# Kernel tuning notes

Hardware: AMD Instinct MI355X
Metric: run time of the kernel (lower is better)

## Reference

```python
import jax, jax.numpy as jnp
import numpy as np

B, L = 2, 1024
D_MODEL = 1024
D_STATE = 16
K = 3            # conv kernel (odd so padding=(K-1)//2 preserves L)
EXPAND = 1       # module is only shape-consistent with d_inner == d_model
D_INNER = D_MODEL * EXPAND


def setup_inputs() -> dict:
    key = jax.random.key(0)
    ks = jax.random.split(key, 10)
    s = 0.02
    x = jax.random.normal(ks[0], (B, L, D_MODEL), dtype=jnp.float32)
    W_in = jax.random.normal(ks[1], (D_MODEL, 2 * D_INNER), dtype=jnp.float32) * s
    conv_w = jax.random.normal(ks[2], (D_INNER, 1, K), dtype=jnp.float32) * s  # depthwise OIH
    W_B = jax.random.normal(ks[3], (D_INNER, D_STATE), dtype=jnp.float32) * s
    W_C = jax.random.normal(ks[4], (D_INNER, D_STATE), dtype=jnp.float32) * s
    W_delta = jax.random.normal(ks[5], (D_INNER, D_MODEL), dtype=jnp.float32) * s
    delta_base = jax.random.normal(ks[6], (D_MODEL,), dtype=jnp.float32)
    W_tau = jax.random.normal(ks[7], (D_MODEL, D_MODEL), dtype=jnp.float32) * s
    A_log = jnp.tile(jnp.log(jnp.arange(1, D_STATE + 1, dtype=jnp.float32)), (D_MODEL, 1))
    W_out = jax.random.normal(ks[8], (D_INNER, D_MODEL), dtype=jnp.float32) * s
    return {"x": x, "W_in": W_in, "conv_w": conv_w, "W_B": W_B, "W_C": W_C,
            "W_delta": W_delta, "delta_base": delta_base, "W_tau": W_tau,
            "A_log": A_log, "W_out": W_out}


def _silu(v):
    return v * jax.nn.sigmoid(v)


def _mamba_fwd(x, W_in, conv_w, W_B, W_C, W_delta, delta_base, W_tau, A_log, W_out):
    residual = x
    z = x @ W_in                               # [B,L,2*D_INNER]
    val, gate = jnp.split(z, 2, axis=-1)
    # depthwise causal-ish conv1d (padding=(K-1)//2)
    v = jnp.transpose(val, (0, 2, 1))          # [B,C,L]
    v = jax.lax.conv_general_dilated(
        v, conv_w, window_strides=(1,), padding=[((K - 1) // 2, (K - 1) // 2)],
        dimension_numbers=("NCH", "OIH", "NCH"), feature_group_count=D_INNER)
    val = jnp.transpose(_silu(v), (0, 2, 1))   # [B,L,D_INNER]

    B_proj = val @ W_B                          # [B,L,N]
    C_proj = val @ W_C                          # [B,L,N]
    combined_delta = val @ W_delta + delta_base # [B,L,D_MODEL]
    Delta = jax.nn.softplus(combined_delta @ W_tau)  # [B,L,D]

    A = -jnp.exp(A_log)                         # [D,N]
    dA = Delta[..., None] * A                   # [B,L,D,N]
    A_bar = jnp.exp(dA)
    B_bar = jnp.expm1(dA) / (dA + 1e-6) * Delta[..., None] * B_proj[:, :, None, :]

    def step(h, inp):
        a_t, b_t, c_t, u_t = inp                # a/b:[B,D,N], c:[B,N], u:[B,D]
        h = a_t * h + b_t * u_t[..., None]
        y_t = jnp.sum(h * c_t[:, None, :], axis=-1)  # [B,D]
        return h, y_t

    h0 = jnp.zeros((x.shape[0], D_INNER, D_STATE), dtype=x.dtype)
    xs = (jnp.moveaxis(A_bar, 1, 0), jnp.moveaxis(B_bar, 1, 0),
          jnp.moveaxis(C_proj, 1, 0), jnp.moveaxis(val, 1, 0))
    _, ys = jax.lax.scan(step, h0, xs)          # ys: [L,B,D]
    y = jnp.moveaxis(ys, 0, 1)                  # [B,L,D]

    out = (y * _silu(gate)) @ W_out + residual  # [B,L,D_MODEL]
    return out


def reference(x, W_in, conv_w, W_B, W_C, W_delta, delta_base, W_tau, A_log, W_out):
    return _mamba_fwd(x, W_in, conv_w, W_B, W_C, W_delta, delta_base, W_tau, A_log, W_out)
```

## Files before the change

kernel.cpp:

```cpp
#include <hip/hip_runtime.h>
#include <math.h>

#define BB 2
#define LL 1024
#define DM 1024
#define DI 1024
#define DS 16
#define ROWS (BB * LL)
#define CH 16
#define NCH (LL / CH)
#define NP 1152

typedef unsigned short ushort_t;
typedef __attribute__((ext_vector_type(8))) short short8;
typedef __attribute__((ext_vector_type(4))) float f32x4;
typedef __attribute__((ext_vector_type(4))) float f4;
typedef __attribute__((ext_vector_type(4))) ushort_t us4;

static __device__ __forceinline__ float sp_f(float x) {
    return fmaxf(x, 0.f) + log1pf(expf(-fabsf(x)));
}
static __device__ __forceinline__ ushort_t f2bf(float f) {
    unsigned u = __float_as_uint(f);
    u += 0x7fffu + ((u >> 16) & 1u);
    return (ushort_t)(u >> 16);
}
static __device__ __forceinline__ float bf2f(ushort_t s) {
    return __uint_as_float(((unsigned)s) << 16);
}

#define SWZ(L) ((L) ^ ((((L) >> 7) & 1) << 4) ^ ((((L) >> 8) & 1) << 5))

template <int ACT, bool HAS_BIAS, bool HAS_RES, bool OUTBF, bool PROJ>
__global__ __launch_bounds__(256) void gemm_bf_k(
    const ushort_t* __restrict__ A, const ushort_t* __restrict__ Bt,
    const float* __restrict__ bias, const float* __restrict__ res,
    void* __restrict__ Cout, float* __restrict__ BpO, float* __restrict__ CpO,
    int M, int N, int K)
{
    __shared__ __align__(16) char lsa[8192];
    __shared__ __align__(16) char lsb[8192];

    const int tid = threadIdx.x;
    const int lane = tid & 63;
    const int w = tid >> 6, wr = w >> 1, wc = w & 1;
    const int row0 = blockIdx.y * 128, col0 = blockIdx.x * 128;
    const int rl = lane & 15, q = lane >> 4;

    const int srow = tid >> 2, schunk = tid & 3;
    const int Pw0 = SWZ(tid * 16);
    const int Pw1 = SWZ(4096 + tid * 16);

    int LA[4], LB[4];
#pragma unroll
    for (int m = 0; m < 4; ++m) LA[m] = SWZ((wr * 64 + m * 16 + rl) * 64 + q * 16);
#pragma unroll
    for (int n = 0; n < 4; ++n) LB[n] = SWZ((wc * 64 + n * 16 + rl) * 64 + q * 16);

    const ushort_t* pA = A + (size_t)(row0 + srow) * K + schunk * 8;
    const ushort_t* pB = Bt + (size_t)(col0 + srow) * K + schunk * 8;
    const size_t rowskip = (size_t)64 * K;

    short8 ra0 = *(const short8*)(pA);
    short8 ra1 = *(const short8*)(pA + rowskip);
    short8 rb0 = *(const short8*)(pB);
    short8 rb1 = *(const short8*)(pB + rowskip);

    f32x4 acc[4][4] = {};

    const int NT = K >> 5;
    for (int kt = 0; kt < NT; ++kt) {
        __syncthreads();
        *(short8*)(lsa + Pw0) = ra0;
        *(short8*)(lsa + Pw1) = ra1;
        *(short8*)(lsb + Pw0) = rb0;
        *(short8*)(lsb + Pw1) = rb1;
        __syncthreads();
        if (kt + 1 < NT) {
            const ushort_t* nA = pA + (size_t)(kt + 1) * 32;
            const ushort_t* nB = pB + (size_t)(kt + 1) * 32;
            ra0 = *(const short8*)(nA);
            ra1 = *(const short8*)(nA + rowskip);
            rb0 = *(const short8*)(nB);
            rb1 = *(const short8*)(nB + rowskip);
        }
        short8 af[4], bfr[4];
#pragma unroll
        for (int m = 0; m < 4; ++m) af[m] = *(const short8*)(lsa + LA[m]);
#pragma unroll
        for (int n = 0; n < 4; ++n) bfr[n] = *(const short8*)(lsb + LB[n]);
#pragma unroll
        for (int m = 0; m < 4; ++m)
#pragma unroll
            for (int n = 0; n < 4; ++n)
                acc[m][n] = __builtin_amdgcn_mfma_f32_16x16x32_bf16(
                    af[m], bfr[n], acc[m][n], 0, 0, 0);
    }

    float bia[4];
#pragma unroll
    for (int n = 0; n < 4; ++n) {
        int c = col0 + wc * 64 + n * 16 + rl;
        bia[n] = (HAS_BIAS && c < DM) ? bias[c] : 0.f;
    }
#pragma unroll
    for (int m = 0; m < 4; ++m) {
#pragma unroll
        for (int n = 0; n < 4; ++n) {
            int c = col0 + wc * 64 + n * 16 + rl;
#pragma unroll
            for (int i = 0; i < 4; ++i) {
                int r = row0 + wr * 64 + m * 16 + q * 4 + i;
                float v = acc[m][n][i];
                if (PROJ && c >= DM) {
                    if (c < DM + DS)          BpO[(size_t)r * DS + (c - DM)] = v;
                    else if (c < DM + 2 * DS) CpO[(size_t)r * DS + (c - DM - DS)] = v;
                } else {
                    v += bia[n];
                    if (ACT == 1) v = sp_f(v);
                    if (HAS_RES) v += res[(size_t)r * N + c];
                    if (OUTBF) ((ushort_t*)Cout)[(size_t)r * N + c] = f2bf(v);
                    else       ((float*)Cout)[(size_t)r * N + c] = v;
                }
            }
        }
    }
}

__global__ __launch_bounds__(256) void tconv_k(
    const float* __restrict__ in, ushort_t* __restrict__ out, int K, int N)
{
    __shared__ float t[32][33];
    int lx = threadIdx.x & 31, ly = threadIdx.x >> 5;
    int n0 = blockIdx.x * 32, k0 = blockIdx.y * 32;
#pragma unroll
    for (int i = 0; i < 32; i += 8)
        t[ly + i][lx] = in[(size_t)(k0 + ly + i) * N + n0 + lx];
    __syncthreads();
#pragma unroll
    for (int i = 0; i < 32; i += 8)
        out[(size_t)(n0 + ly + i) * K + k0 + lx] = f2bf(t[lx][ly + i]);
}

__global__ __launch_bounds__(256) void tail_pack_k(
    const float* __restrict__ WB, const float* __restrict__ WC,
    ushort_t* __restrict__ WdcT)
{
    int t = blockIdx.x * 256 + threadIdx.x;
    int k = t & (DM - 1);
    int r = t >> 10;
    ushort_t v = 0;
    if (r < DS)          v = f2bf(WB[(size_t)k * DS + r]);
    else if (r < 2 * DS) v = f2bf(WC[(size_t)k * DS + (r - DS)]);
    WdcT[(size_t)(DM + r) * DM + k] = v;
}

__global__ __launch_bounds__(256) void cvt_bf_k(
    const float* __restrict__ in, ushort_t* __restrict__ out)
{
    int t = blockIdx.x * 256 + threadIdx.x;
    f4 v = ((const f4*)in)[t];
    us4 o;
    o.x = f2bf(v.x); o.y = f2bf(v.y); o.z = f2bf(v.z); o.w = f2bf(v.w);
    ((us4*)out)[t] = o;
}

__global__ __launch_bounds__(256) void conv_silu_k(
    const ushort_t* __restrict__ z_bf, const float* __restrict__ cw,
    ushort_t* __restrict__ val_bf)
{
    int t = blockIdx.x * 256 + threadIdx.x;
    int c0 = (t & 255) * 4;
    int row = t >> 8;
    int l = row & (LL - 1);
    const ushort_t* zr = z_bf + (size_t)row * (2 * DI) + c0;
    us4 zz = {0, 0, 0, 0};
    us4 vm = (l > 0)      ? *(const us4*)(zr - 2 * DI) : zz;
    us4 v0 = *(const us4*)(zr);
    us4 vp = (l < LL - 1) ? *(const us4*)(zr + 2 * DI) : zz;
    const f4* wp = (const f4*)(cw + (size_t)c0 * 3);
    f4 w0 = wp[0], w1 = wp[1], w2 = wp[2];
    float w[12];
#pragma unroll
    for (int k = 0; k < 4; ++k) { w[k] = w0[k]; w[4 + k] = w1[k]; w[8 + k] = w2[k]; }
    us4 o;
#pragma unroll
    for (int j = 0; j < 4; ++j) {
        float s = bf2f(vm[j]) * w[3 * j] + bf2f(v0[j]) * w[3 * j + 1]
                + bf2f(vp[j]) * w[3 * j + 2];
        float si = s / (1.f + __expf(-s));
        o[j] = f2bf(si);
    }
    *(us4*)(val_bf + (size_t)row * DI + c0) = o;
}

__global__ __launch_bounds__(256) void scan_p1_k(
    const ushort_t* __restrict__ Del_bf, const ushort_t* __restrict__ val_bf,
    const float* __restrict__ Bp, const float* __restrict__ A_log,
    float* __restrict__ aprod, float* __restrict__ hloc)
{
    int t = blockIdx.x * 256 + threadIdx.x;
    int d = t & (DI - 1);
    int c = (t >> 10) & (NCH - 1);
    int b = t >> 16;

    float Adn[DS], ci[DS];
    const f4* alp = (const f4*)(A_log + (size_t)d * DS);
#pragma unroll
    for (int j = 0; j < 4; ++j) {
        f4 al = alp[j];
#pragma unroll
        for (int k = 0; k < 4; ++k) {
            float a = -__expf(al[k]);
            Adn[j * 4 + k] = a;
            ci[j * 4 + k] = 1.0f / a;
        }
    }
    int row0 = b * LL + c * CH;
    const ushort_t* Dp = Del_bf + (size_t)row0 * DI + d;
    const ushort_t* up = val_bf + (size_t)row0 * DI + d;
    const f4* bp = (const f4*)(Bp + (size_t)row0 * DS);

    float h[DS];
#pragma unroll
    for (int n = 0; n < DS; ++n) h[n] = 0.f;
    float sdv = 0.f;

#pragma unroll 2
    for (int l = 0; l < CH; ++l) {
        float dv = bf2f(Dp[(size_t)l * DI]);
        float u  = bf2f(up[(size_t)l * DI]);
        f4 q0 = bp[l * 4 + 0], q1 = bp[l * 4 + 1], q2 = bp[l * 4 + 2], q3 = bp[l * 4 + 3];
        float bn[DS];
#pragma unroll
        for (int k = 0; k < 4; ++k) {
            bn[k] = q0[k]; bn[4 + k] = q1[k]; bn[8 + k] = q2[k]; bn[12 + k] = q3[k];
        }
        sdv += dv;
#pragma unroll
        for (int n = 0; n < DS; ++n) {
            float a  = __expf(dv * Adn[n]);
            float tt = (ci[n] * bn[n]) * u;
            float s  = h[n] + tt;
            h[n] = fmaf(a, s, -tt);
        }
    }
    size_t o = (((size_t)b * NCH + c) * DI + d) * DS;
#pragma unroll
    for (int j = 0; j < 4; ++j) {
        f4 hv, av;
#pragma unroll
        for (int k = 0; k < 4; ++k) {
            hv[k] = h[j * 4 + k];
            av[k] = __expf(sdv * Adn[j * 4 + k]);
        }
        *(f4*)(hloc + o + j * 4) = hv;
        *(f4*)(aprod + o + j * 4) = av;
    }
}

__global__ __launch_bounds__(256) void scan_p2_k(
    const float* __restrict__ aprod, const float* __restrict__ hloc,
    float* __restrict__ hin)
{
    int t = blockIdx.x * 256 + threadIdx.x;
    int dn = t & (DI * DS - 1);
    int b = t >> 14;
    float h = 0.f;
    size_t base = (size_t)b * NCH * DI * DS + dn;
#pragma unroll 4
    for (int c = 0; c < NCH; ++c) {
        size_t idx = base + (size_t)c * (DI * DS);
        hin[idx] = h;
        h = fmaf(aprod[idx], h, hloc[idx]);
    }
}

__global__ __launch_bounds__(256) void scan_p3_k(
    const ushort_t* __restrict__ Del_bf, const ushort_t* __restrict__ val_bf,
    const float* __restrict__ Bp, const float* __restrict__ Cp,
    const float* __restrict__ A_log, const float* __restrict__ hin,
    const ushort_t* __restrict__ z_bf, ushort_t* __restrict__ g_bf)
{
    int t = blockIdx.x * 256 + threadIdx.x;
    int d = t & (DI - 1);
    int c = (t >> 10) & (NCH - 1);
    int b = t >> 16;

    float Adn[DS], ci[DS];
    const f4* alp = (const f4*)(A_log + (size_t)d * DS);
#pragma unroll
    for (int j = 0; j < 4; ++j) {
        f4 al = alp[j];
#pragma unroll
        for (int k = 0; k < 4; ++k) {
            float a = -__expf(al[k]);
            Adn[j * 4 + k] = a;
            ci[j * 4 + k] = 1.0f / a;
        }
    }
    int row0 = b * LL + c * CH;
    const ushort_t* Dp = Del_bf + (size_t)row0 * DI + d;
    const ushort_t* up = val_bf + (size_t)row0 * DI + d;
    const ushort_t* zp = z_bf + (size_t)row0 * (2 * DI) + DI + d;
    const f4* bp = (const f4*)(Bp + (size_t)row0 * DS);
    const f4* cp = (const f4*)(Cp + (size_t)row0 * DS);
    ushort_t* gp = g_bf + (size_t)row0 * DI + d;

    float h[DS];
    size_t o = (((size_t)b * NCH + c) * DI + d) * DS;
#pragma unroll
    for (int j = 0; j < 4; ++j) {
        f4 hv = *(const f4*)(hin + o + j * 4);
#pragma unroll
        for (int k = 0; k < 4; ++k) h[j * 4 + k] = hv[k];
    }

#pragma unroll 2
    for (int l = 0; l < CH; ++l) {
        float dv = bf2f(Dp[(size_t)l * DI]);
        float u  = bf2f(up[(size_t)l * DI]);
        f4 q0 = bp[l * 4 + 0], q1 = bp[l * 4 + 1], q2 = bp[l * 4 + 2], q3 = bp[l * 4 + 3];
        f4 r0 = cp[l * 4 + 0], r1 = cp[l * 4 + 1], r2 = cp[l * 4 + 2], r3 = cp[l * 4 + 3];
        float bn[DS], cn[DS];
#pragma unroll
        for (int k = 0; k < 4; ++k) {
            bn[k] = q0[k]; bn[4 + k] = q1[k]; bn[8 + k] = q2[k]; bn[12 + k] = q3[k];
            cn[k] = r0[k]; cn[4 + k] = r1[k]; cn[8 + k] = r2[k]; cn[12 + k] = r3[k];
        }
        float psum = 0.f;
#pragma unroll
        for (int n = 0; n < DS; ++n) {
            float a  = __expf(dv * Adn[n]);
            float tt = (ci[n] * bn[n]) * u;
            float s  = h[n] + tt;
            h[n] = fmaf(a, s, -tt);
            psum = fmaf(h[n], cn[n], psum);
        }
        float zg = bf2f(zp[(size_t)l * 2 * DI]);
        float si = zg / (1.f + __expf(-zg));
        gp[(size_t)l * DI] = f2bf(psum * si);
    }
}

extern "C" void kernel_launch(void* const* d_in, const int* in_sizes, int n_in,
                              void* d_out, int out_size, void* d_ws, size_t ws_size,
                              hipStream_t stream)
{
    (void)in_sizes; (void)n_in; (void)out_size; (void)ws_size;

    const float* x        = (const float*)d_in[0];
    const float* W_in     = (const float*)d_in[1];
    const float* conv_w   = (const float*)d_in[2];
    const float* W_B      = (const float*)d_in[3];
    const float* W_C      = (const float*)d_in[4];
    const float* W_delta  = (const float*)d_in[5];
    const float* delta_b  = (const float*)d_in[6];
    const float* W_tau    = (const float*)d_in[7];
    const float* A_log    = (const float*)d_in[8];
    const float* W_out    = (const float*)d_in[9];
    float* out = (float*)d_out;

    const size_t M1 = 1024 * 1024;
    ushort_t* us = (ushort_t*)d_ws;
    ushort_t* z_bf   = us;
    ushort_t* val_bf = us + 4 * M1;
    ushort_t* cmb_bf = us + 6 * M1;
    ushort_t* Del_bf = us + 8 * M1;
    ushort_t* x_bf   = us + 10 * M1;
    ushort_t* g_bf   = us + 12 * M1;
    ushort_t* WinT   = us + 14 * M1;
    ushort_t* WdcT   = us + 16 * M1;
    ushort_t* WtT    = us + 16 * M1 + (size_t)NP * DM;
    ushort_t* WoT    = WtT + M1;
    float* fb   = (float*)(us + 20 * M1);
    float* Bp    = fb;
    float* Cp    = fb + (size_t)ROWS * DS;
    float* aprod = fb + 2 * (size_t)ROWS * DS;
    float* hloc  = aprod + 2 * M1;
    float* hin   = hloc + 2 * M1;

    cvt_bf_k<<<(ROWS * DM / 4) / 256, 256, 0, stream>>>(x, x_bf);
    tconv_k<<<dim3(2 * DI / 32, DM / 32), 256, 0, stream>>>(W_in, WinT, DM, 2 * DI);
    tconv_k<<<dim3(DM / 32, DI / 32), 256, 0, stream>>>(W_delta, WdcT, DI, DM);
    tail_pack_k<<<(128 * DM) / 256, 256, 0, stream>>>(W_B, W_C, WdcT);
    tconv_k<<<dim3(DM / 32, DM / 32), 256, 0, stream>>>(W_tau, WtT, DM, DM);
    tconv_k<<<dim3(DM / 32, DI / 32), 256, 0, stream>>>(W_out, WoT, DI, DM);

    gemm_bf_k<0, false, false, true, false><<<dim3(2 * DI / 128, ROWS / 128), 256, 0, stream>>>(
        x_bf, WinT, nullptr, nullptr, z_bf, nullptr, nullptr, ROWS, 2 * DI, DM);

    conv_silu_k<<<(ROWS * DI / 4) / 256, 256, 0, stream>>>(z_bf, conv_w, val_bf);

    gemm_bf_k<0, true, false, true, true><<<dim3(NP / 128, ROWS / 128), 256, 0, stream>>>(
        val_bf, WdcT, delta_b, nullptr, cmb_bf, Bp, Cp, ROWS, NP, DI);

    gemm_bf_k<1, false, false, true, false><<<dim3(DM / 128, ROWS / 128), 256, 0, stream>>>(
        cmb_bf, WtT, nullptr, nullptr, Del_bf, nullptr, nullptr, ROWS, DM, DM);

    scan_p1_k<<<(BB * NCH * DI) / 256, 256, 0, stream>>>(
        Del_bf, val_bf, Bp, A_log, aprod, hloc);
    scan_p2_k<<<(BB * DI * DS) / 256, 256, 0, stream>>>(aprod, hloc, hin);
    scan_p3_k<<<(BB * NCH * DI) / 256, 256, 0, stream>>>(
        Del_bf, val_bf, Bp, Cp, A_log, hin, z_bf, g_bf);

    gemm_bf_k<0, false, true, false, false><<<dim3(DM / 128, ROWS / 128), 256, 0, stream>>>(
        g_bf, WoT, nullptr, x, out, nullptr, nullptr, ROWS, DM, DI);
}
```

Before: 256.4 us.

## Fold W_delta·W_tau into one weight, double-buffer GEMM via direct global-to-LDS loads

Precomputes the product of W_delta and W_tau (plus a folded bias delta_base·W_tau) per call, so the two chained activation GEMMs become a single GEMM with softplus, with B/C projections still appended as extra columns. The GEMM kernel now uses global_load_lds into double-buffered shared memory with one barrier per k-step, and is templated on the N tile width so some GEMMs use 64-wide tiles for more blocks. This removes an ROWS×DM×DM GEMM and an intermediate buffer at the cost of a DM³ weight GEMM each call and extra bf16 rounding of the fused weight.

```diff
diff --git a/kernel.cpp b/kernel.cpp
--- a/kernel.cpp
+++ b/kernel.cpp
@@ -9,7 +9,7 @@
 #define ROWS (BB * LL)
 #define CH 16
 #define NCH (LL / CH)
-#define NP 1152
+#define NP 1088
 
 typedef unsigned short ushort_t;
 typedef __attribute__((ext_vector_type(8))) short short8;
@@ -31,83 +31,99 @@
 
 #define SWZ(L) ((L) ^ ((((L) >> 7) & 1) << 4) ^ ((((L) >> 8) & 1) << 5))
 
-template <int ACT, bool HAS_BIAS, bool HAS_RES, bool OUTBF, bool PROJ>
+static __device__ __forceinline__ void gl_lds16(const void* g, void* l) {
+    __builtin_amdgcn_global_load_lds(
+        (const __attribute__((address_space(1))) unsigned int*)g,
+        (__attribute__((address_space(3))) unsigned int*)l, 16, 0, 0);
+}
+
+template <int TN, int ACT, bool HAS_BIAS, bool HAS_RES, bool OUTBF, bool PROJ>
 __global__ __launch_bounds__(256) void gemm_bf_k(
     const ushort_t* __restrict__ A, const ushort_t* __restrict__ Bt,
     const float* __restrict__ bias, const float* __restrict__ res,
     void* __restrict__ Cout, float* __restrict__ BpO, float* __restrict__ CpO,
-    int M, int N, int K)
-{
-    __shared__ __align__(16) char lsa[8192];
-    __shared__ __align__(16) char lsb[8192];
+    int M, int N, int K, int ldc)
+{
+    constexpr int NACC = TN / 32;
+    constexpr int BCH = TN / 64;
+    __shared__ __align__(16) char lsa[2][8192];
+    __shared__ __align__(16) char lsb[2][TN * 64];
 
     const int tid = threadIdx.x;
     const int lane = tid & 63;
-    const int w = tid >> 6, wr = w >> 1, wc = w & 1;
-    const int row0 = blockIdx.y * 128, col0 = blockIdx.x * 128;
+    const int w = tid >> 6;
+    const int wr = w >> 1, wc = w & 1;
+    const int row0 = blockIdx.y * 128, col0 = blockIdx.x * TN;
     const int rl = lane & 15, q = lane >> 4;
 
-    const int srow = tid >> 2, schunk = tid & 3;
-    const int Pw0 = SWZ(tid * 16);
-    const int Pw1 = SWZ(4096 + tid * 16);
-
-    int LA[4], LB[4];
+    const char* gA[2];
+#pragma unroll
+    for (int j = 0; j < 2; ++j) {
+        int Lc = (w * 2 + j) * 1024 + lane * 16;
+        int L = SWZ(Lc);
+        gA[j] = (const char*)A + ((size_t)(row0 + (L >> 6)) * K) * 2 + (L & 63);
+    }
+    const char* gB[BCH];
+#pragma unroll
+    for (int j = 0; j < BCH; ++j) {
+        int Lc = (w * BCH + j) * 1024 + lane * 16;
+        int L = SWZ(Lc);
+        gB[j] = (const char*)Bt + ((size_t)(col0 + (L >> 6)) * K) * 2 + (L & 63);
+    }
+
+    int LA[4], LB[NACC];
 #pragma unroll
     for (int m = 0; m < 4; ++m) LA[m] = SWZ((wr * 64 + m * 16 + rl) * 64 + q * 16);
 #pragma unroll
-    for (int n = 0; n < 4; ++n) LB[n] = SWZ((wc * 64 + n * 16 + rl) * 64 + q * 16);
-
-    const ushort_t* pA = A + (size_t)(row0 + srow) * K + schunk * 8;
-    const ushort_t* pB = Bt + (size_t)(col0 + srow) * K + schunk * 8;
-    const size_t rowskip = (size_t)64 * K;
-
-    short8 ra0 = *(const short8*)(pA);
-    short8 ra1 = *(const short8*)(pA + rowskip);
-    short8 rb0 = *(const short8*)(pB);
-    short8 rb1 = *(const short8*)(pB + rowskip);
-
-    f32x4 acc[4][4] = {};
-
+    for (int n = 0; n < NACC; ++n)
+        LB[n] = SWZ((wc * (TN / 2) + n * 16 + rl) * 64 + q * 16);
+
+    f32x4 acc[4][NACC] = {};
     const int NT = K >> 5;
+
+#pragma unroll
+    for (int j = 0; j < 2; ++j) gl_lds16(gA[j], &lsa[0][(w * 2 + j) * 1024]);
+#pragma unroll
+    for (int j = 0; j < BCH; ++j) gl_lds16(gB[j], &lsb[0][(w * BCH + j) * 1024]);
+    __syncthreads();
+
+    int cur = 0;
     for (int kt = 0; kt < NT; ++kt) {
-        __syncthreads();
-        *(short8*)(lsa + Pw0) = ra0;
-        *(short8*)(lsa + Pw1) = ra1;
-        *(short8*)(lsb + Pw0) = rb0;
-        *(short8*)(lsb + Pw1) = rb1;
-        __syncthreads();
         if (kt + 1 < NT) {
-            const ushort_t* nA = pA + (size_t)(kt + 1) * 32;
-            const ushort_t* nB = pB + (size_t)(kt + 1) * 32;
-            ra0 = *(const short8*)(nA);
-            ra1 = *(const short8*)(nA + rowskip);
-            rb0 = *(const short8*)(nB);
-            rb1 = *(const short8*)(nB + rowskip);
-        }
-        short8 af[4], bfr[4];
-#pragma unroll
-        for (int m = 0; m < 4; ++m) af[m] = *(const short8*)(lsa + LA[m]);
-#pragma unroll
-        for (int n = 0; n < 4; ++n) bfr[n] = *(const short8*)(lsb + LB[n]);
+            const int kb = (kt + 1) * 64;
+#pragma unroll
+            for (int j = 0; j < 2; ++j)
+                gl_lds16(gA[j] + kb, &lsa[cur ^ 1][(w * 2 + j) * 1024]);
+#pragma unroll
+            for (int j = 0; j < BCH; ++j)
+                gl_lds16(gB[j] + kb, &lsb[cur ^ 1][(w * BCH + j) * 1024]);
+        }
+        short8 af[4], bfr[NACC];
+#pragma unroll
+        for (int m = 0; m < 4; ++m) af[m] = *(const short8*)(&lsa[cur][LA[m]]);
+#pragma unroll
+        for (int n = 0; n < NACC; ++n) bfr[n] = *(const short8*)(&lsb[cur][LB[n]]);
 #pragma unroll
         for (int m = 0; m < 4; ++m)
 #pragma unroll
-            for (int n = 0; n < 4; ++n)
+            for (int n = 0; n < NACC; ++n)
                 acc[m][n] = __builtin_amdgcn_mfma_f32_16x16x32_bf16(
                     af[m], bfr[n], acc[m][n], 0, 0, 0);
-    }
-
-    float bia[4];
-#pragma unroll
-    for (int n = 0; n < 4; ++n) {
-        int c = col0 + wc * 64 + n * 16 + rl;
+        __syncthreads();
+        cur ^= 1;
+    }
+
+    float bia[NACC];
+#pragma unroll
+    for (int n = 0; n < NACC; ++n) {
+        int c = col0 + wc * (TN / 2) + n * 16 + rl;
         bia[n] = (HAS_BIAS && c < DM) ? bias[c] : 0.f;
     }
 #pragma unroll
     for (int m = 0; m < 4; ++m) {
 #pragma unroll
-        for (int n = 0; n < 4; ++n) {
-            int c = col0 + wc * 64 + n * 16 + rl;
+        for (int n = 0; n < NACC; ++n) {
+            int c = col0 + wc * (TN / 2) + n * 16 + rl;
 #pragma unroll
             for (int i = 0; i < 4; ++i) {
                 int r = row0 + wr * 64 + m * 16 + q * 4 + i;
@@ -118,9 +134,9 @@
                 } else {
                     v += bia[n];
                     if (ACT == 1) v = sp_f(v);
-                    if (HAS_RES) v += res[(size_t)r * N + c];
-                    if (OUTBF) ((ushort_t*)Cout)[(size_t)r * N + c] = f2bf(v);
-                    else       ((float*)Cout)[(size_t)r * N + c] = v;
+                    if (HAS_RES) v += res[(size_t)r * ldc + c];
+                    if (OUTBF) ((ushort_t*)Cout)[(size_t)r * ldc + c] = f2bf(v);
+                    else       ((float*)Cout)[(size_t)r * ldc + c] = v;
                 }
             }
         }
@@ -153,6 +169,17 @@
     if (r < DS)          v = f2bf(WB[(size_t)k * DS + r]);
     else if (r < 2 * DS) v = f2bf(WC[(size_t)k * DS + (r - DS)]);
     WdcT[(size_t)(DM + r) * DM + k] = v;
+}
+
+__global__ __launch_bounds__(256) void bias2_k(
+    const float* __restrict__ db, const float* __restrict__ Wt,
+    float* __restrict__ b2)
+{
+    int n = blockIdx.x * 256 + threadIdx.x;
+    float s = 0.f;
+#pragma unroll 4
+    for (int m = 0; m < DM; ++m) s = fmaf(db[m], Wt[(size_t)m * DM + n], s);
+    b2[n] = s;
 }
 
 __global__ __launch_bounds__(256) void cvt_bf_k(
@@ -365,38 +392,40 @@
     ushort_t* us = (ushort_t*)d_ws;
     ushort_t* z_bf   = us;
     ushort_t* val_bf = us + 4 * M1;
-    ushort_t* cmb_bf = us + 6 * M1;
-    ushort_t* Del_bf = us + 8 * M1;
-    ushort_t* x_bf   = us + 10 * M1;
-    ushort_t* g_bf   = us + 12 * M1;
-    ushort_t* WinT   = us + 14 * M1;
-    ushort_t* WdcT   = us + 16 * M1;
-    ushort_t* WtT    = us + 16 * M1 + (size_t)NP * DM;
-    ushort_t* WoT    = WtT + M1;
-    float* fb   = (float*)(us + 20 * M1);
+    ushort_t* Del_bf = us + 6 * M1;
+    ushort_t* x_bf   = us + 8 * M1;
+    ushort_t* g_bf   = us + 10 * M1;
+    ushort_t* WinT   = us + 12 * M1;
+    ushort_t* WoT    = us + 14 * M1;
+    ushort_t* WtT    = us + 15 * M1;
+    ushort_t* Wd_bf  = us + 16 * M1;
+    ushort_t* WdcT   = us + 17 * M1;
+    float* fb    = (float*)(us + 20 * M1);
     float* Bp    = fb;
     float* Cp    = fb + (size_t)ROWS * DS;
-    float* aprod = fb + 2 * (size_t)ROWS * DS;
+    float* bias2 = fb + 2 * (size_t)ROWS * DS;
+    float* aprod = bias2 + 1024;
     float* hloc  = aprod + 2 * M1;
     float* hin   = hloc + 2 * M1;
 
     cvt_bf_k<<<(ROWS * DM / 4) / 256, 256, 0, stream>>>(x, x_bf);
+    cvt_bf_k<<<(DI * DM / 4) / 256, 256, 0, stream>>>(W_delta, Wd_bf);
     tconv_k<<<dim3(2 * DI / 32, DM / 32), 256, 0, stream>>>(W_in, WinT, DM, 2 * DI);
-    tconv_k<<<dim3(DM / 32, DI / 32), 256, 0, stream>>>(W_delta, WdcT, DI, DM);
-    tail_pack_k<<<(128 * DM) / 256, 256, 0, stream>>>(W_B, W_C, WdcT);
     tconv_k<<<dim3(DM / 32, DM / 32), 256, 0, stream>>>(W_tau, WtT, DM, DM);
     tconv_k<<<dim3(DM / 32, DI / 32), 256, 0, stream>>>(W_out, WoT, DI, DM);
-
-    gemm_bf_k<0, false, false, true, false><<<dim3(2 * DI / 128, ROWS / 128), 256, 0, stream>>>(
-        x_bf, WinT, nullptr, nullptr, z_bf, nullptr, nullptr, ROWS, 2 * DI, DM);
+    tail_pack_k<<<(64 * DM) / 256, 256, 0, stream>>>(W_B, W_C, WdcT);
+    bias2_k<<<DM / 256, 256, 0, stream>>>(delta_b, W_tau, bias2);
+
+    gemm_bf_k<64, 0, false, false, true, false><<<dim3(DM / 64, DI / 128), 256, 0, stream>>>(
+        WtT, Wd_bf, nullptr, nullptr, WdcT, nullptr, nullptr, DM, DI, DM, DM);
+
+    gemm_bf_k<128, 0, false, false, true, false><<<dim3(2 * DI / 128, ROWS / 128), 256, 0, stream>>>(
+        x_bf, WinT, nullptr, nullptr, z_bf, nullptr, nullptr, ROWS, 2 * DI, DM, 2 * DI);
 
     conv_silu_k<<<(ROWS * DI / 4) / 256, 256, 0, stream>>>(z_bf, conv_w, val_bf);
 
-    gemm_bf_k<0, true, false, true, true><<<dim3(NP / 128, ROWS / 128), 256, 0, stream>>>(
-        val_bf, WdcT, delta_b, nullptr, cmb_bf, Bp, Cp, ROWS, NP, DI);
-
-    gemm_bf_k<1, false, false, true, false><<<dim3(DM / 128, ROWS / 128), 256, 0, stream>>>(
-        cmb_bf, WtT, nullptr, nullptr, Del_bf, nullptr, nullptr, ROWS, DM, DM);
+    gemm_bf_k<64, 1, true, false, true, true><<<dim3(NP / 64, ROWS / 128), 256, 0, stream>>>(
+        val_bf, WdcT, bias2, nullptr, Del_bf, Bp, Cp, ROWS, NP, DI, DM);
 
     scan_p1_k<<<(BB * NCH * DI) / 256, 256, 0, stream>>>(
         Del_bf, val_bf, Bp, A_log, aprod, hloc);
@@ -404,6 +433,6 @@
     scan_p3_k<<<(BB * NCH * DI) / 256, 256, 0, stream>>>(
         Del_bf, val_bf, Bp, Cp, A_log, hin, z_bf, g_bf);
 
-    gemm_bf_k<0, false, true, false, false><<<dim3(DM / 128, ROWS / 128), 256, 0, stream>>>(
-        g_bf, WoT, nullptr, x, out, nullptr, nullptr, ROWS, DM, DI);
-}
+    gemm_bf_k<64, 0, false, true, false, false><<<dim3(DM / 64, ROWS / 128), 256, 0, stream>>>(
+        g_bf, WoT, nullptr, x, out, nullptr, nullptr, ROWS, DM, DI, DM);
+}
```

New measurement: 339.7 us. 1.32x slower.
